# Performance work log

Measured on AMD Instinct MI355X. Metric: run time of the kernel, lower is better.

Reference implementation:

```python
import jax, jax.numpy as jnp
import numpy as np
from jax import lax

J2 = -1.0
J4 = 0.5
KT = 0.5
DT = 0.01
SIGMA = float(np.sqrt(2.0 * KT * DT))  # noise scale per Euler-Maruyama step


def setup_inputs() -> dict:
    key = jax.random.key(0)
    k_x, = jax.random.split(key, 1)
    n_samples, n_dim = 2048, 256
    x0 = jax.random.normal(k_x, (n_samples, n_dim), dtype=jnp.float32)
    b = jnp.zeros((n_dim,), dtype=jnp.float32)  # learned bias parameter
    return {"x0": x0, "b": b, "n_steps": 500}


def reference(x0, b, n_steps):
    # Langevin dynamics: x <- x - grad_V(x)*dt + sqrt(2 kT dt)*N(0,1)
    # grad_V(x) = 2*J2*x + 4*J4*x^3 + b
    keys = jax.random.split(jax.random.key(1), n_steps)

    def step(x, k):
        grad = 2.0 * J2 * x + 4.0 * J4 * x * x * x + b
        noise = jax.random.normal(k, x.shape, x.dtype) * SIGMA
        return x - grad * DT + noise, None

    x, _ = lax.scan(step, x0, keys)
    return x
```

## Files before the change

kernel.cpp:

```cpp
#include <hip/hip_runtime.h>


__device__ __forceinline__ float sconst(float v) {
  return __uint_as_float(__builtin_amdgcn_readfirstlane(__float_as_uint(v)));
}

__device__ __forceinline__ void tf2x32(unsigned k0, unsigned k1,
                                       unsigned c0, unsigned c1,
                                       unsigned& o0, unsigned& o1) {
  const unsigned k2 = k0 ^ k1 ^ 0x1BD11BDAu;
  unsigned x0 = c0 + k0, x1 = c1 + k1;
#define TF1(R) x0 += x1; x1 = ((x1 << (R)) | (x1 >> (32 - (R)))); x1 ^= x0;
  TF1(13) TF1(15) TF1(26) TF1(6)  x0 += k1; x1 += k2 + 1u;
  TF1(17) TF1(29) TF1(16) TF1(24) x0 += k2; x1 += k0 + 2u;
  TF1(13) TF1(15) TF1(26) TF1(6)  x0 += k0; x1 += k1 + 3u;
  TF1(17) TF1(29) TF1(16) TF1(24) x0 += k1; x1 += k2 + 4u;
  TF1(13) TF1(15) TF1(26) TF1(6)  x0 += k2; x1 += k0 + 5u;
#undef TF1
  o0 = x0; o1 = x1;
}

__device__ __forceinline__ void tf_fold2k(uint4 ka, uint4 kb, unsigned cj,
                                          unsigned& ra, unsigned& rb) {
  unsigned a0 = ka.x, a1 = cj + ka.y;
  unsigned b0 = kb.x, b1 = cj + kb.y;
#define TFR2(R)                                   \
  a0 += a1; b0 += b1;                             \
  a1 = ((a1 << (R)) | (a1 >> (32 - (R)))) ^ a0;   \
  b1 = ((b1 << (R)) | (b1 >> (32 - (R)))) ^ b0;
  TFR2(13) TFR2(15) TFR2(26) TFR2(6)
  a0 += ka.y; b0 += kb.y; a1 = a1 + ka.z + 1u; b1 = b1 + kb.z + 1u;
  TFR2(17) TFR2(29) TFR2(16) TFR2(24)
  a0 += ka.z; b0 += kb.z; a1 = a1 + ka.x + 2u; b1 = b1 + kb.x + 2u;
  TFR2(13) TFR2(15) TFR2(26) TFR2(6)
  a0 += ka.x; b0 += kb.x; a1 = a1 + ka.y + 3u; b1 = b1 + kb.y + 3u;
  TFR2(17) TFR2(29) TFR2(16) TFR2(24)
  a0 += ka.y; b0 += kb.y; a1 = a1 + ka.z + 4u; b1 = b1 + kb.z + 4u;
  TFR2(13) TFR2(15) TFR2(26) TFR2(6)
  a0 += ka.z; b0 += kb.z; a1 = a1 + ka.x + 5u; b1 = b1 + kb.x + 5u;
#undef TFR2
  ra = a0 ^ a1;
  rb = b0 ^ b1;
}

__global__ __launch_bounds__(256, 8) void langevin_tf(
    const float* __restrict__ x0p, const float* __restrict__ bias,
    const int* __restrict__ nsteps_p, float* __restrict__ out,
    int N, int ndim) {
  __shared__ __align__(16) uint4 skeys[512];
  const int n_steps = __builtin_amdgcn_readfirstlane(nsteps_p[0]);
  const int nfill = n_steps < 512 ? n_steps : 512;
  for (int l = (int)threadIdx.x; l < nfill; l += (int)blockDim.x) {
    unsigned o0, o1;
    tf2x32(0u, 1u, 0u, (unsigned)l, o0, o1);
    skeys[l] = make_uint4(o0, o1, o0 ^ o1 ^ 0x1BD11BDAu, 0u);
  }
  __syncthreads();

  const int j = (int)(blockIdx.x * blockDim.x + threadIdx.x);
  if (j >= N) return;
  const unsigned cj = (unsigned)j;
  float x = x0p[j];
  const float b = bias[j % ndim];

  const float LO = sconst(-0.99999994f);
  const float NLN2 = sconst(-0.693147180559945f);
  const float C8 = sconst(2.81022636e-08f), C7 = sconst(3.43273939e-07f);
  const float C6 = sconst(-3.5233877e-06f), C5 = sconst(-4.39150654e-06f);
  const float C4 = sconst(0.00021858087f),  C3 = sconst(-0.00125372503f);
  const float C2 = sconst(-0.00417768164f), C1 = sconst(0.246640727f);
  const float C0 = sconst(1.50140941f);
  const float T8 = sconst(-0.000200214257f), T7 = sconst(0.000100950558f);
  const float T6 = sconst(0.00134934322f),   T5 = sconst(-0.00367342844f);
  const float T4 = sconst(0.00573950773f),   T3 = sconst(-0.0076224613f);
  const float T2 = sconst(0.00943887047f),   T1 = sconst(1.00167406f);
  const float T0 = sconst(2.83297682f);
  const float CS = sconst(0.1f * __uint_as_float(0x3FB504F3u));
  const float A1 = sconst(1.02f);
  const float A3 = sconst(-0.02f);
  const float bp = b * -0.01f;

  if (n_steps <= 512) {
    int t = 0;
#pragma unroll 1
    for (; t + 1 < n_steps; t += 2) {
      const uint4 ka = skeys[t];
      const uint4 kb = skeys[t + 1];
      unsigned ra, rb;
      tf_fold2k(ka, kb, cj, ra, rb);
      const float fa = __uint_as_float((ra >> 9) | 0x3F800000u) - 1.0f;
      const float fb = __uint_as_float((rb >> 9) | 0x3F800000u) - 1.0f;
      const float ua = fmaf(fa, 2.0f, LO);
      const float ub = fmaf(fb, 2.0f, LO);
      const float wa = __log2f(1.0f - ua * ua) * NLN2;
      const float wb = __log2f(1.0f - ub * ub) * NLN2;
      const float za = wa - 2.5f;
      const float zb = wb - 2.5f;
      float pa = C8, pb = C8;
      pa = fmaf(pa, za, C7); pb = fmaf(pb, zb, C7);
      pa = fmaf(pa, za, C6); pb = fmaf(pb, zb, C6);
      pa = fmaf(pa, za, C5); pb = fmaf(pb, zb, C5);
      pa = fmaf(pa, za, C4); pb = fmaf(pb, zb, C4);
      pa = fmaf(pa, za, C3); pb = fmaf(pb, zb, C3);
      pa = fmaf(pa, za, C2); pb = fmaf(pb, zb, C2);
      pa = fmaf(pa, za, C1); pb = fmaf(pb, zb, C1);
      pa = fmaf(pa, za, C0); pb = fmaf(pb, zb, C0);
      float ea = pa * ua;
      float eb = pb * ub;
      if (__any((wa >= 5.0f) | (wb >= 5.0f))) {
        const float qza = __builtin_amdgcn_sqrtf(wa) - 3.0f;
        const float qzb = __builtin_amdgcn_sqrtf(wb) - 3.0f;
        float qa = T8, qb = T8;
        qa = fmaf(qa, qza, T7); qb = fmaf(qb, qzb, T7);
        qa = fmaf(qa, qza, T6); qb = fmaf(qb, qzb, T6);
        qa = fmaf(qa, qza, T5); qb = fmaf(qb, qzb, T5);
        qa = fmaf(qa, qza, T4); qb = fmaf(qb, qzb, T4);
        qa = fmaf(qa, qza, T3); qb = fmaf(qb, qzb, T3);
        qa = fmaf(qa, qza, T2); qb = fmaf(qb, qzb, T2);
        qa = fmaf(qa, qza, T1); qb = fmaf(qb, qzb, T1);
        qa = fmaf(qa, qza, T0); qb = fmaf(qb, qzb, T0);
        ea = (wa >= 5.0f) ? qa * ua : ea;
        eb = (wb >= 5.0f) ? qb * ub : eb;
      }
      float x3 = (x * x) * x;
      x = fmaf(x, A1, fmaf(x3, A3, fmaf(ea, CS, bp)));
      x3 = (x * x) * x;
      x = fmaf(x, A1, fmaf(x3, A3, fmaf(eb, CS, bp)));
    }
    if (t < n_steps) {
      const uint4 ka = skeys[t];
      unsigned ra, rb;
      tf_fold2k(ka, ka, cj, ra, rb);
      const float fa = __uint_as_float((ra >> 9) | 0x3F800000u) - 1.0f;
      const float ua = fmaf(fa, 2.0f, LO);
      const float wa = __log2f(1.0f - ua * ua) * NLN2;
      float pa, za;
      if (wa < 5.0f) { za = wa - 2.5f;
        pa = C8; pa = fmaf(pa, za, C7); pa = fmaf(pa, za, C6);
        pa = fmaf(pa, za, C5); pa = fmaf(pa, za, C4); pa = fmaf(pa, za, C3);
        pa = fmaf(pa, za, C2); pa = fmaf(pa, za, C1); pa = fmaf(pa, za, C0);
      } else { za = __builtin_amdgcn_sqrtf(wa) - 3.0f;
        pa = T8; pa = fmaf(pa, za, T7); pa = fmaf(pa, za, T6);
        pa = fmaf(pa, za, T5); pa = fmaf(pa, za, T4); pa = fmaf(pa, za, T3);
        pa = fmaf(pa, za, T2); pa = fmaf(pa, za, T1); pa = fmaf(pa, za, T0);
      }
      const float ea = pa * ua;
      const float x3 = (x * x) * x;
      x = fmaf(x, A1, fmaf(x3, A3, fmaf(ea, CS, bp)));
    }
  } else {
    for (int t = 0; t < n_steps; ++t) {
      unsigned o0, o1;
      tf2x32(0u, 1u, 0u, (unsigned)t, o0, o1);
      const uint4 ka = make_uint4(o0, o1, o0 ^ o1 ^ 0x1BD11BDAu, 0u);
      unsigned ra, rb;
      tf_fold2k(ka, ka, cj, ra, rb);
      const float fa = __uint_as_float((ra >> 9) | 0x3F800000u) - 1.0f;
      const float ua = fmaf(fa, 2.0f, LO);
      const float wa = __log2f(1.0f - ua * ua) * NLN2;
      float pa, za;
      if (wa < 5.0f) { za = wa - 2.5f;
        pa = C8; pa = fmaf(pa, za, C7); pa = fmaf(pa, za, C6);
        pa = fmaf(pa, za, C5); pa = fmaf(pa, za, C4); pa = fmaf(pa, za, C3);
        pa = fmaf(pa, za, C2); pa = fmaf(pa, za, C1); pa = fmaf(pa, za, C0);
      } else { za = __builtin_amdgcn_sqrtf(wa) - 3.0f;
        pa = T8; pa = fmaf(pa, za, T7); pa = fmaf(pa, za, T6);
        pa = fmaf(pa, za, T5); pa = fmaf(pa, za, T4); pa = fmaf(pa, za, T3);
        pa = fmaf(pa, za, T2); pa = fmaf(pa, za, T1); pa = fmaf(pa, za, T0);
      }
      const float ea = pa * ua;
      const float x3 = (x * x) * x;
      x = fmaf(x, A1, fmaf(x3, A3, fmaf(ea, CS, bp)));
    }
  }
  out[j] = x;
}

extern "C" void kernel_launch(void* const* d_in, const int* in_sizes, int n_in,
                              void* d_out, int out_size, void* d_ws, size_t ws_size,
                              hipStream_t stream) {
  (void)n_in; (void)d_ws; (void)ws_size; (void)out_size;
  const float* x0 = (const float*)d_in[0];
  const float* b = (const float*)d_in[1];
  const int* ns = (const int*)d_in[2];
  float* out = (float*)d_out;

  const int n = in_sizes[0];
  const int ndim = in_sizes[1];
  const int block = 256;
  const int grid = (n + block - 1) / block;
  hipLaunchKernelGGL(langevin_tf, dim3(grid), dim3(block), 0, stream,
                     x0, b, ns, out, n, ndim);
}
```

Baseline: 573.5 us.

## Move per-step keys to workspace and stream them via scalar loads

Per-step Threefry keys are now generated once by a separate small keygen kernel into the workspace buffer. The main kernel reads them with double-buffered inline-asm s_load_dwordx4 into SGPRs, so the keys are wave-uniform scalars instead of LDS reads into VGPRs, and it processes four steps per loop iteration. This drops the per-block LDS fill and barrier and frees vector registers and LDS bandwidth in the hot loop. The cost is an extra kernel launch, reliance on the workspace buffer, and inline asm whose waitcnt handling must be correct. The prefetch reads up to four keys past the last step used, which stays inside the 512-entry table only because of the 508-step cap.

```diff
diff --git a/kernel.cpp b/kernel.cpp
--- a/kernel.cpp
+++ b/kernel.cpp
@@ -1,5 +1,7 @@
 #include <hip/hip_runtime.h>
 
+
+typedef unsigned v4u __attribute__((ext_vector_type(4)));
 
 __device__ __forceinline__ float sconst(float v) {
   return __uint_as_float(__builtin_amdgcn_readfirstlane(__float_as_uint(v)));
@@ -20,158 +22,158 @@
   o0 = x0; o1 = x1;
 }
 
-__device__ __forceinline__ void tf_fold2k(uint4 ka, uint4 kb, unsigned cj,
+__device__ __forceinline__ void tf_fold2k(v4u ka, v4u kb, unsigned cj,
                                           unsigned& ra, unsigned& rb) {
-  unsigned a0 = ka.x, a1 = cj + ka.y;
-  unsigned b0 = kb.x, b1 = cj + kb.y;
+  unsigned a0 = ka[0], a1 = cj + ka[1];
+  unsigned b0 = kb[0], b1 = cj + kb[1];
 #define TFR2(R)                                   \
   a0 += a1; b0 += b1;                             \
   a1 = ((a1 << (R)) | (a1 >> (32 - (R)))) ^ a0;   \
   b1 = ((b1 << (R)) | (b1 >> (32 - (R)))) ^ b0;
   TFR2(13) TFR2(15) TFR2(26) TFR2(6)
-  a0 += ka.y; b0 += kb.y; a1 = a1 + ka.z + 1u; b1 = b1 + kb.z + 1u;
+  a0 += ka[1]; b0 += kb[1]; a1 = a1 + ka[2] + 1u; b1 = b1 + kb[2] + 1u;
   TFR2(17) TFR2(29) TFR2(16) TFR2(24)
-  a0 += ka.z; b0 += kb.z; a1 = a1 + ka.x + 2u; b1 = b1 + kb.x + 2u;
+  a0 += ka[2]; b0 += kb[2]; a1 = a1 + ka[0] + 2u; b1 = b1 + kb[0] + 2u;
   TFR2(13) TFR2(15) TFR2(26) TFR2(6)
-  a0 += ka.x; b0 += kb.x; a1 = a1 + ka.y + 3u; b1 = b1 + kb.y + 3u;
+  a0 += ka[0]; b0 += kb[0]; a1 = a1 + ka[1] + 3u; b1 = b1 + kb[1] + 3u;
   TFR2(17) TFR2(29) TFR2(16) TFR2(24)
-  a0 += ka.y; b0 += kb.y; a1 = a1 + ka.z + 4u; b1 = b1 + kb.z + 4u;
+  a0 += ka[1]; b0 += kb[1]; a1 = a1 + ka[2] + 4u; b1 = b1 + kb[2] + 4u;
   TFR2(13) TFR2(15) TFR2(26) TFR2(6)
-  a0 += ka.z; b0 += kb.z; a1 = a1 + ka.x + 5u; b1 = b1 + kb.x + 5u;
+  a0 += ka[2]; b0 += kb[2]; a1 = a1 + ka[0] + 5u; b1 = b1 + kb[0] + 5u;
 #undef TFR2
   ra = a0 ^ a1;
   rb = b0 ^ b1;
 }
 
-__global__ __launch_bounds__(256, 8) void langevin_tf(
-    const float* __restrict__ x0p, const float* __restrict__ bias,
-    const int* __restrict__ nsteps_p, float* __restrict__ out,
-    int N, int ndim) {
-  __shared__ __align__(16) uint4 skeys[512];
-  const int n_steps = __builtin_amdgcn_readfirstlane(nsteps_p[0]);
-  const int nfill = n_steps < 512 ? n_steps : 512;
-  for (int l = (int)threadIdx.x; l < nfill; l += (int)blockDim.x) {
+__global__ void keygen(uint4* __restrict__ kw) {
+  const int l = (int)(blockIdx.x * blockDim.x + threadIdx.x);
+  if (l < 512) {
     unsigned o0, o1;
     tf2x32(0u, 1u, 0u, (unsigned)l, o0, o1);
-    skeys[l] = make_uint4(o0, o1, o0 ^ o1 ^ 0x1BD11BDAu, 0u);
-  }
-  __syncthreads();
-
+    kw[l] = make_uint4(o0, o1, o0 ^ o1 ^ 0x1BD11BDAu, 0u);
+  }
+}
+
+#define NORM2_UPDATE(ra, rb)                                                 \
+  {                                                                          \
+    const float fa = __uint_as_float(((ra) >> 9) | 0x3F800000u) - 1.0f;      \
+    const float fb = __uint_as_float(((rb) >> 9) | 0x3F800000u) - 1.0f;      \
+    const float ua = fmaf(fa, 2.0f, LO);                                     \
+    const float ub = fmaf(fb, 2.0f, LO);                                     \
+    const float wa = __log2f(1.0f - ua * ua) * NLN2;                         \
+    const float wb = __log2f(1.0f - ub * ub) * NLN2;                         \
+    const float za = wa - 2.5f;                                              \
+    const float zb = wb - 2.5f;                                              \
+    float pa = C8, pb = C8;                                                  \
+    pa = fmaf(pa, za, C7); pb = fmaf(pb, zb, C7);                            \
+    pa = fmaf(pa, za, C6); pb = fmaf(pb, zb, C6);                            \
+    pa = fmaf(pa, za, C5); pb = fmaf(pb, zb, C5);                            \
+    pa = fmaf(pa, za, C4); pb = fmaf(pb, zb, C4);                            \
+    pa = fmaf(pa, za, C3); pb = fmaf(pb, zb, C3);                            \
+    pa = fmaf(pa, za, C2); pb = fmaf(pb, zb, C2);                            \
+    pa = fmaf(pa, za, C1); pb = fmaf(pb, zb, C1);                            \
+    pa = fmaf(pa, za, C0); pb = fmaf(pb, zb, C0);                            \
+    float ea = pa * ua;                                                      \
+    float eb = pb * ub;                                                      \
+    if (__any((wa >= 5.0f) | (wb >= 5.0f))) {                 \
+      const float qza = __builtin_amdgcn_sqrtf(wa) - 3.0f;                   \
+      const float qzb = __builtin_amdgcn_sqrtf(wb) - 3.0f;                   \
+      float qa = T8, qb = T8;                                                \
+      qa = fmaf(qa, qza, T7); qb = fmaf(qb, qzb, T7);                        \
+      qa = fmaf(qa, qza, T6); qb = fmaf(qb, qzb, T6);                        \
+      qa = fmaf(qa, qza, T5); qb = fmaf(qb, qzb, T5);                        \
+      qa = fmaf(qa, qza, T4); qb = fmaf(qb, qzb, T4);                        \
+      qa = fmaf(qa, qza, T3); qb = fmaf(qb, qzb, T3);                        \
+      qa = fmaf(qa, qza, T2); qb = fmaf(qb, qzb, T2);                        \
+      qa = fmaf(qa, qza, T1); qb = fmaf(qb, qzb, T1);                        \
+      qa = fmaf(qa, qza, T0); qb = fmaf(qb, qzb, T0);                        \
+      ea = (wa >= 5.0f) ? qa * ua : ea;                                      \
+      eb = (wb >= 5.0f) ? qb * ub : eb;                                      \
+    }                                                                        \
+    float x3 = (x * x) * x;                                                  \
+    x = fmaf(x, A1, fmaf(x3, A3, fmaf(ea, CS, bp)));                         \
+    x3 = (x * x) * x;                                                        \
+    x = fmaf(x, A1, fmaf(x3, A3, fmaf(eb, CS, bp)));                         \
+  }
+
+#define DECL_CONSTS                                                          \
+  const float LO = sconst(-0.99999994f);                                     \
+  const float NLN2 = sconst(-0.693147180559945f);                            \
+  const float C8 = sconst(2.81022636e-08f), C7 = sconst(3.43273939e-07f);    \
+  const float C6 = sconst(-3.5233877e-06f), C5 = sconst(-4.39150654e-06f);   \
+  const float C4 = sconst(0.00021858087f),  C3 = sconst(-0.00125372503f);    \
+  const float C2 = sconst(-0.00417768164f), C1 = sconst(0.246640727f);       \
+  const float C0 = sconst(1.50140941f);                                      \
+  const float T8 = sconst(-0.000200214257f), T7 = sconst(0.000100950558f);   \
+  const float T6 = sconst(0.00134934322f),   T5 = sconst(-0.00367342844f);   \
+  const float T4 = sconst(0.00573950773f),   T3 = sconst(-0.0076224613f);    \
+  const float T2 = sconst(0.00943887047f),   T1 = sconst(1.00167406f);       \
+  const float T0 = sconst(2.83297682f);                                      \
+  const float CS = sconst(0.1f * __uint_as_float(0x3FB504F3u));              \
+  const float A1 = sconst(1.02f);                                            \
+  const float A3 = sconst(-0.02f);
+
+__global__ __launch_bounds__(256, 8) void langevin_sk(
+    const float* __restrict__ x0p, const float* __restrict__ bias,
+    const int* __restrict__ nsteps_p, const uint4* __restrict__ kw,
+    float* __restrict__ out, int N, int ndim) {
+  const int n_steps = __builtin_amdgcn_readfirstlane(nsteps_p[0]);
   const int j = (int)(blockIdx.x * blockDim.x + threadIdx.x);
   if (j >= N) return;
   const unsigned cj = (unsigned)j;
   float x = x0p[j];
   const float b = bias[j % ndim];
-
-  const float LO = sconst(-0.99999994f);
-  const float NLN2 = sconst(-0.693147180559945f);
-  const float C8 = sconst(2.81022636e-08f), C7 = sconst(3.43273939e-07f);
-  const float C6 = sconst(-3.5233877e-06f), C5 = sconst(-4.39150654e-06f);
-  const float C4 = sconst(0.00021858087f),  C3 = sconst(-0.00125372503f);
-  const float C2 = sconst(-0.00417768164f), C1 = sconst(0.246640727f);
-  const float C0 = sconst(1.50140941f);
-  const float T8 = sconst(-0.000200214257f), T7 = sconst(0.000100950558f);
-  const float T6 = sconst(0.00134934322f),   T5 = sconst(-0.00367342844f);
-  const float T4 = sconst(0.00573950773f),   T3 = sconst(-0.0076224613f);
-  const float T2 = sconst(0.00943887047f),   T1 = sconst(1.00167406f);
-  const float T0 = sconst(2.83297682f);
-  const float CS = sconst(0.1f * __uint_as_float(0x3FB504F3u));
-  const float A1 = sconst(1.02f);
-  const float A3 = sconst(-0.02f);
+  DECL_CONSTS
   const float bp = b * -0.01f;
 
-  if (n_steps <= 512) {
-    int t = 0;
+  const int n4 = (n_steps <= 508) ? (n_steps & ~3) : 0;
+  const uint4* kp = kw;
+  v4u k0a, k0b, k1a, k1b;
+  if (n4 > 0) {
+    asm volatile("s_load_dwordx4 %0, %2, 0x0\n\t"
+                 "s_load_dwordx4 %1, %2, 0x10\n\t"
+                 "s_waitcnt lgkmcnt(0)"
+                 : "=&s"(k0a), "=&s"(k0b) : "s"(kp));
+  }
 #pragma unroll 1
-    for (; t + 1 < n_steps; t += 2) {
-      const uint4 ka = skeys[t];
-      const uint4 kb = skeys[t + 1];
-      unsigned ra, rb;
-      tf_fold2k(ka, kb, cj, ra, rb);
-      const float fa = __uint_as_float((ra >> 9) | 0x3F800000u) - 1.0f;
-      const float fb = __uint_as_float((rb >> 9) | 0x3F800000u) - 1.0f;
-      const float ua = fmaf(fa, 2.0f, LO);
-      const float ub = fmaf(fb, 2.0f, LO);
-      const float wa = __log2f(1.0f - ua * ua) * NLN2;
-      const float wb = __log2f(1.0f - ub * ub) * NLN2;
-      const float za = wa - 2.5f;
-      const float zb = wb - 2.5f;
-      float pa = C8, pb = C8;
-      pa = fmaf(pa, za, C7); pb = fmaf(pb, zb, C7);
-      pa = fmaf(pa, za, C6); pb = fmaf(pb, zb, C6);
-      pa = fmaf(pa, za, C5); pb = fmaf(pb, zb, C5);
-      pa = fmaf(pa, za, C4); pb = fmaf(pb, zb, C4);
-      pa = fmaf(pa, za, C3); pb = fmaf(pb, zb, C3);
-      pa = fmaf(pa, za, C2); pb = fmaf(pb, zb, C2);
-      pa = fmaf(pa, za, C1); pb = fmaf(pb, zb, C1);
-      pa = fmaf(pa, za, C0); pb = fmaf(pb, zb, C0);
-      float ea = pa * ua;
-      float eb = pb * ub;
-      if (__any((wa >= 5.0f) | (wb >= 5.0f))) {
-        const float qza = __builtin_amdgcn_sqrtf(wa) - 3.0f;
-        const float qzb = __builtin_amdgcn_sqrtf(wb) - 3.0f;
-        float qa = T8, qb = T8;
-        qa = fmaf(qa, qza, T7); qb = fmaf(qb, qzb, T7);
-        qa = fmaf(qa, qza, T6); qb = fmaf(qb, qzb, T6);
-        qa = fmaf(qa, qza, T5); qb = fmaf(qb, qzb, T5);
-        qa = fmaf(qa, qza, T4); qb = fmaf(qb, qzb, T4);
-        qa = fmaf(qa, qza, T3); qb = fmaf(qb, qzb, T3);
-        qa = fmaf(qa, qza, T2); qb = fmaf(qb, qzb, T2);
-        qa = fmaf(qa, qza, T1); qb = fmaf(qb, qzb, T1);
-        qa = fmaf(qa, qza, T0); qb = fmaf(qb, qzb, T0);
-        ea = (wa >= 5.0f) ? qa * ua : ea;
-        eb = (wb >= 5.0f) ? qb * ub : eb;
-      }
-      float x3 = (x * x) * x;
-      x = fmaf(x, A1, fmaf(x3, A3, fmaf(ea, CS, bp)));
-      x3 = (x * x) * x;
-      x = fmaf(x, A1, fmaf(x3, A3, fmaf(eb, CS, bp)));
+  for (int t = 0; t < n4; t += 4) {
+    asm volatile("s_load_dwordx4 %0, %2, 0x20\n\t"
+                 "s_load_dwordx4 %1, %2, 0x30"
+                 : "=&s"(k1a), "=&s"(k1b) : "s"(kp));
+    unsigned ra, rb;
+    tf_fold2k(k0a, k0b, cj, ra, rb);
+    NORM2_UPDATE(ra, rb)
+    asm volatile("s_waitcnt lgkmcnt(0)" : "+s"(k1a), "+s"(k1b));
+    asm volatile("s_load_dwordx4 %0, %2, 0x40\n\t"
+                 "s_load_dwordx4 %1, %2, 0x50"
+                 : "=&s"(k0a), "=&s"(k0b) : "s"(kp));
+    tf_fold2k(k1a, k1b, cj, ra, rb);
+    NORM2_UPDATE(ra, rb)
+    asm volatile("s_waitcnt lgkmcnt(0)" : "+s"(k0a), "+s"(k0b));
+    kp += 4;
+  }
+  for (int t = n4; t < n_steps; ++t) {
+    unsigned o0, o1;
+    tf2x32(0u, 1u, 0u, (unsigned)t, o0, o1);
+    v4u ka = {o0, o1, o0 ^ o1 ^ 0x1BD11BDAu, 0u};
+    unsigned ra, rb;
+    tf_fold2k(ka, ka, cj, ra, rb);
+    const float fa = __uint_as_float((ra >> 9) | 0x3F800000u) - 1.0f;
+    const float ua = fmaf(fa, 2.0f, LO);
+    const float wa = __log2f(1.0f - ua * ua) * NLN2;
+    float pa, za;
+    if (wa < 5.0f) { za = wa - 2.5f;
+      pa = C8; pa = fmaf(pa, za, C7); pa = fmaf(pa, za, C6);
+      pa = fmaf(pa, za, C5); pa = fmaf(pa, za, C4); pa = fmaf(pa, za, C3);
+      pa = fmaf(pa, za, C2); pa = fmaf(pa, za, C1); pa = fmaf(pa, za, C0);
+    } else { za = __builtin_amdgcn_sqrtf(wa) - 3.0f;
+      pa = T8; pa = fmaf(pa, za, T7); pa = fmaf(pa, za, T6);
+      pa = fmaf(pa, za, T5); pa = fmaf(pa, za, T4); pa = fmaf(pa, za, T3);
+      pa = fmaf(pa, za, T2); pa = fmaf(pa, za, T1); pa = fmaf(pa, za, T0);
     }
-    if (t < n_steps) {
-      const uint4 ka = skeys[t];
-      unsigned ra, rb;
-      tf_fold2k(ka, ka, cj, ra, rb);
-      const float fa = __uint_as_float((ra >> 9) | 0x3F800000u) - 1.0f;
-      const float ua = fmaf(fa, 2.0f, LO);
-      const float wa = __log2f(1.0f - ua * ua) * NLN2;
-      float pa, za;
-      if (wa < 5.0f) { za = wa - 2.5f;
-        pa = C8; pa = fmaf(pa, za, C7); pa = fmaf(pa, za, C6);
-        pa = fmaf(pa, za, C5); pa = fmaf(pa, za, C4); pa = fmaf(pa, za, C3);
-        pa = fmaf(pa, za, C2); pa = fmaf(pa, za, C1); pa = fmaf(pa, za, C0);
-      } else { za = __builtin_amdgcn_sqrtf(wa) - 3.0f;
-        pa = T8; pa = fmaf(pa, za, T7); pa = fmaf(pa, za, T6);
-        pa = fmaf(pa, za, T5); pa = fmaf(pa, za, T4); pa = fmaf(pa, za, T3);
-        pa = fmaf(pa, za, T2); pa = fmaf(pa, za, T1); pa = fmaf(pa, za, T0);
-      }
-      const float ea = pa * ua;
-      const float x3 = (x * x) * x;
-      x = fmaf(x, A1, fmaf(x3, A3, fmaf(ea, CS, bp)));
-    }
-  } else {
-    for (int t = 0; t < n_steps; ++t) {
-      unsigned o0, o1;
-      tf2x32(0u, 1u, 0u, (unsigned)t, o0, o1);
-      const uint4 ka = make_uint4(o0, o1, o0 ^ o1 ^ 0x1BD11BDAu, 0u);
-      unsigned ra, rb;
-      tf_fold2k(ka, ka, cj, ra, rb);
-      const float fa = __uint_as_float((ra >> 9) | 0x3F800000u) - 1.0f;
-      const float ua = fmaf(fa, 2.0f, LO);
-      const float wa = __log2f(1.0f - ua * ua) * NLN2;
-      float pa, za;
-      if (wa < 5.0f) { za = wa - 2.5f;
-        pa = C8; pa = fmaf(pa, za, C7); pa = fmaf(pa, za, C6);
-        pa = fmaf(pa, za, C5); pa = fmaf(pa, za, C4); pa = fmaf(pa, za, C3);
-        pa = fmaf(pa, za, C2); pa = fmaf(pa, za, C1); pa = fmaf(pa, za, C0);
-      } else { za = __builtin_amdgcn_sqrtf(wa) - 3.0f;
-        pa = T8; pa = fmaf(pa, za, T7); pa = fmaf(pa, za, T6);
-        pa = fmaf(pa, za, T5); pa = fmaf(pa, za, T4); pa = fmaf(pa, za, T3);
-        pa = fmaf(pa, za, T2); pa = fmaf(pa, za, T1); pa = fmaf(pa, za, T0);
-      }
-      const float ea = pa * ua;
-      const float x3 = (x * x) * x;
-      x = fmaf(x, A1, fmaf(x3, A3, fmaf(ea, CS, bp)));
-    }
+    const float ea = pa * ua;
+    const float x3 = (x * x) * x;
+    x = fmaf(x, A1, fmaf(x3, A3, fmaf(ea, CS, bp)));
   }
   out[j] = x;
 }
@@ -179,7 +181,7 @@
 extern "C" void kernel_launch(void* const* d_in, const int* in_sizes, int n_in,
                               void* d_out, int out_size, void* d_ws, size_t ws_size,
                               hipStream_t stream) {
-  (void)n_in; (void)d_ws; (void)ws_size; (void)out_size;
+  (void)n_in; (void)out_size;
   const float* x0 = (const float*)d_in[0];
   const float* b = (const float*)d_in[1];
   const int* ns = (const int*)d_in[2];
@@ -187,8 +189,12 @@
 
   const int n = in_sizes[0];
   const int ndim = in_sizes[1];
+  uint4* kw = (uint4*)d_ws;
+  (void)ws_size;
+
+  hipLaunchKernelGGL(keygen, dim3(2), dim3(256), 0, stream, kw);
   const int block = 256;
   const int grid = (n + block - 1) / block;
-  hipLaunchKernelGGL(langevin_tf, dim3(grid), dim3(block), 0, stream,
-                     x0, b, ns, out, n, ndim);
-}
+  hipLaunchKernelGGL(langevin_sk, dim3(grid), dim3(block), 0, stream,
+                     x0, b, ns, kw, out, n, ndim);
+}
```

Result: no change. 579.5 us (+1.0%).
